# Optimization experiments

Measured on AMD Instinct MI355X. Metric: run time of the kernel, lower is better.

## Reference

```python
import jax, jax.numpy as jnp
import numpy as np


def setup_inputs() -> dict:
    key = jax.random.key(0)
    k1, k2, k3 = jax.random.split(key, 3)
    Lq, Lkv, H, D = 2048, 2048, 16, 128
    return {
        "query": jax.random.normal(k1, (Lq, H, D), dtype=jnp.float32),
        "key": jax.random.normal(k2, (Lkv, H, D), dtype=jnp.float32),
        "value": jax.random.normal(k3, (Lkv, H, D), dtype=jnp.float32),
    }


def reference(query, key, value):
    # query: [Lq, H, D], key: [Lkv, H, D], value: [Lkv, H, Dv]
    # Original module performs chunked online-softmax attention; the math is
    # exactly scaled-dot-product softmax attention with scale 1/sqrt(k_features).
    d = query.shape[-1]
    q = query * (1.0 / jnp.sqrt(jnp.asarray(d, dtype=query.dtype)))
    scores = jnp.einsum('qhd,khd->qhk', q, key)          # [Lq, H, Lkv]
    weights = jax.nn.softmax(scores, axis=-1)            # numerically stable online softmax equivalent
    out = jnp.einsum('qhk,khf->qhf', weights, value)     # [Lq, H, Dv]
    return out
```

## Files before the change

kernel.cpp:

```cpp
#include <hip/hip_runtime.h>
#include <hip/hip_bf16.h>

typedef __bf16 bf16x8 __attribute__((ext_vector_type(8)));
typedef __bf16 bf16x4 __attribute__((ext_vector_type(4)));
typedef float  f32x16 __attribute__((ext_vector_type(16)));
typedef float  f32x4  __attribute__((ext_vector_type(4)));

#define HD     2048
#define DH     128
#define KVB    32
#define NSPLIT 2
#define NROWS  32768
#define VSTR   36

template<bool SPLIT>
__global__ __launch_bounds__(256, 2)
void fmha_kern(const float* __restrict__ Qg, const float* __restrict__ Kg,
               const float* __restrict__ Vg, float* __restrict__ outp,
               float* __restrict__ wsML)
{
    __shared__ __align__(16) __bf16 klds[2][32 * 128];
    __shared__ __align__(16) __bf16 vtlds[2][DH * VSTR];

    const int tid  = threadIdx.x;
    const int lane = tid & 63;
    const int wrp  = tid >> 6;
    const int g    = lane >> 5;
    const int l31  = lane & 31;

    const int b = blockIdx.x;
    int h, qblk, sp, t0, nch;
    if constexpr (SPLIT) {
        const int grp = b & 31;
        qblk = b >> 5;
        h    = grp >> 1;
        sp   = grp & 1;
        t0   = sp * 32;
        nch  = 32;
    } else {
        h    = 2 * (b & 7) + ((b >> 3) >> 4);
        qblk = (b >> 3) & 15;
        sp   = 0;
        t0   = 0;
        nch  = 64;
    }

    const float qscale = 1.4426950408889634f * 0.08838834764831845f;
    const int q = qblk * 128 + wrp * 32 + l31;

    bf16x8 qf[8];
    {
        const float* qrow = Qg + (size_t)q * HD + h * DH;
        #pragma unroll
        for (int db = 0; db < 8; ++db) {
            f32x4 a = *(const f32x4*)(qrow + db * 16 + 8 * g);
            f32x4 c = *(const f32x4*)(qrow + db * 16 + 8 * g + 4);
            bf16x8 f;
            f[0] = (__bf16)(a[0] * qscale); f[1] = (__bf16)(a[1] * qscale);
            f[2] = (__bf16)(a[2] * qscale); f[3] = (__bf16)(a[3] * qscale);
            f[4] = (__bf16)(c[0] * qscale); f[5] = (__bf16)(c[1] * qscale);
            f[6] = (__bf16)(c[2] * qscale); f[7] = (__bf16)(c[3] * qscale);
            qf[db] = f;
        }
    }

    const int krow = tid >> 3, kc = tid & 7;
    const int vkv  = tid & 31, vdv0 = (tid >> 5) * 16;
    const float* kbase = Kg + (size_t)h * DH;
    const float* vbase = Vg + (size_t)h * DH;

    f32x4 kreg0, kreg1, kreg2, kreg3, vreg0, vreg1, vreg2, vreg3;

    auto stage_load = [&](int t) {
        const float* kp = kbase + (size_t)(t * KVB + krow) * HD + kc * 8;
        kreg0 = *(const f32x4*)(kp);
        kreg1 = *(const f32x4*)(kp + 4);
        kreg2 = *(const f32x4*)(kp + 64);
        kreg3 = *(const f32x4*)(kp + 68);
        const float* vp = vbase + (size_t)(t * KVB + vkv) * HD + vdv0;
        vreg0 = *(const f32x4*)(vp);
        vreg1 = *(const f32x4*)(vp + 4);
        vreg2 = *(const f32x4*)(vp + 8);
        vreg3 = *(const f32x4*)(vp + 12);
    };

    auto stage_write = [&](int buf) {
        bf16x8 k0, k1;
        k0[0]=(__bf16)kreg0[0]; k0[1]=(__bf16)kreg0[1]; k0[2]=(__bf16)kreg0[2]; k0[3]=(__bf16)kreg0[3];
        k0[4]=(__bf16)kreg1[0]; k0[5]=(__bf16)kreg1[1]; k0[6]=(__bf16)kreg1[2]; k0[7]=(__bf16)kreg1[3];
        k1[0]=(__bf16)kreg2[0]; k1[1]=(__bf16)kreg2[1]; k1[2]=(__bf16)kreg2[2]; k1[3]=(__bf16)kreg2[3];
        k1[4]=(__bf16)kreg3[0]; k1[5]=(__bf16)kreg3[1]; k1[6]=(__bf16)kreg3[2]; k1[7]=(__bf16)kreg3[3];
        const int swz = (krow & 7) << 3;
        *(bf16x8*)&klds[buf][krow * 128 + ((kc * 8) ^ swz)]      = k0;
        *(bf16x8*)&klds[buf][krow * 128 + ((kc * 8 + 64) ^ swz)] = k1;
        #pragma unroll
        for (int jj = 0; jj < 4; ++jj) {
            f32x4 vv = (jj == 0) ? vreg0 : (jj == 1) ? vreg1 : (jj == 2) ? vreg2 : vreg3;
            #pragma unroll
            for (int e = 0; e < 4; ++e)
                vtlds[buf][(vdv0 + jj * 4 + e) * VSTR + vkv] = (__bf16)vv[e];
        }
    };

    auto block_sync = []() {
        asm volatile("s_waitcnt lgkmcnt(0)" ::: "memory");
        __builtin_amdgcn_s_barrier();
    };

    float mrun = -1e30f, lrun = 0.0f;
    f32x16 o0, o1, o2, o3;
    #pragma unroll
    for (int r = 0; r < 16; ++r) { o0[r] = 0.f; o1[r] = 0.f; o2[r] = 0.f; o3[r] = 0.f; }

    stage_load(t0);
    stage_write(0);
    stage_load(t0 + 1);
    block_sync();

    #pragma unroll 2
    for (int tt = 0; tt < nch; ++tt) {
        const int cur = tt & 1;

        f32x16 sa, sb;
        #pragma unroll
        for (int r = 0; r < 16; ++r) { sa[r] = 0.f; sb[r] = 0.f; }
        const int kswz = (l31 & 7) << 3;
        #pragma unroll
        for (int db = 0; db < 4; ++db) {
            bf16x8 kfa = *(const bf16x8*)&klds[cur][l31 * 128 + (((2*db)   * 16 + g * 8) ^ kswz)];
            sa = __builtin_amdgcn_mfma_f32_32x32x16_bf16(kfa, qf[2*db],   sa, 0, 0, 0);
            bf16x8 kfb = *(const bf16x8*)&klds[cur][l31 * 128 + (((2*db+1) * 16 + g * 8) ^ kswz)];
            sb = __builtin_amdgcn_mfma_f32_32x32x16_bf16(kfb, qf[2*db+1], sb, 0, 0, 0);
        }
        f32x16 s;
        #pragma unroll
        for (int r = 0; r < 16; ++r) s[r] = sa[r] + sb[r];

        float m8[8];
        #pragma unroll
        for (int r = 0; r < 8; ++r) m8[r] = fmaxf(s[r], s[r + 8]);
        float tmax = fmaxf(fmaxf(fmaxf(m8[0], m8[4]), fmaxf(m8[1], m8[5])),
                           fmaxf(fmaxf(m8[2], m8[6]), fmaxf(m8[3], m8[7])));
        tmax = fmaxf(tmax, __shfl_xor(tmax, 32, 64));

        if (__any(tmax > mrun + 8.0f)) {
            const float mnew  = fmaxf(mrun, tmax);
            const float alpha = __builtin_amdgcn_exp2f(mrun - mnew);
            lrun *= alpha;
            #pragma unroll
            for (int r = 0; r < 16; ++r) { o0[r] *= alpha; o1[r] *= alpha; o2[r] *= alpha; o3[r] *= alpha; }
            mrun = mnew;
        }

        float p[16];
        #pragma unroll
        for (int r = 0; r < 16; ++r) p[r] = __builtin_amdgcn_exp2f(s[r] - mrun);
        float ps0 = 0, ps1 = 0, ps2 = 0, ps3 = 0;
        #pragma unroll
        for (int r = 0; r < 4; ++r) { ps0 += p[r]; ps1 += p[r+4]; ps2 += p[r+8]; ps3 += p[r+12]; }
        lrun += ((ps0 + ps1) + (ps2 + ps3));

        bf16x8 pf0, pf1;
        #pragma unroll
        for (int e = 0; e < 8; ++e) { pf0[e] = (__bf16)p[e]; pf1[e] = (__bf16)p[8 + e]; }

        #pragma unroll
        for (int bb = 0; bb < 4; ++bb) {
            const __bf16* vb = &vtlds[cur][(bb * 32 + l31) * VSTR];
            bf16x4 a0 = *(const bf16x4*)(vb + 4 * g);
            bf16x4 a1 = *(const bf16x4*)(vb + 8 + 4 * g);
            bf16x8 va;
            va[0]=a0[0]; va[1]=a0[1]; va[2]=a0[2]; va[3]=a0[3];
            va[4]=a1[0]; va[5]=a1[1]; va[6]=a1[2]; va[7]=a1[3];
            f32x16& oo = (bb == 0) ? o0 : (bb == 1) ? o1 : (bb == 2) ? o2 : o3;
            oo = __builtin_amdgcn_mfma_f32_32x32x16_bf16(va, pf0, oo, 0, 0, 0);
            bf16x4 b0 = *(const bf16x4*)(vb + 16 + 4 * g);
            bf16x4 b1 = *(const bf16x4*)(vb + 24 + 4 * g);
            va[0]=b0[0]; va[1]=b0[1]; va[2]=b0[2]; va[3]=b0[3];
            va[4]=b1[0]; va[5]=b1[1]; va[6]=b1[2]; va[7]=b1[3];
            oo = __builtin_amdgcn_mfma_f32_32x32x16_bf16(va, pf1, oo, 0, 0, 0);
        }

        if (tt + 1 < nch) {
            stage_write(cur ^ 1);
            if (tt + 2 < nch) stage_load(t0 + tt + 2);
            block_sync();
        }
    }

    const float ltot  = lrun + __shfl_xor(lrun, 32, 64);
    const int   rowid = q * 16 + h;

    if constexpr (SPLIT) {
        float* orow = outp + ((size_t)sp * NROWS + rowid) * 128;
        #pragma unroll
        for (int bb = 0; bb < 4; ++bb) {
            const f32x16& oo = (bb == 0) ? o0 : (bb == 1) ? o1 : (bb == 2) ? o2 : o3;
            #pragma unroll
            for (int jj = 0; jj < 4; ++jj) {
                f32x4 v;
                v[0] = oo[4*jj+0]; v[1] = oo[4*jj+1]; v[2] = oo[4*jj+2]; v[3] = oo[4*jj+3];
                *(f32x4*)(orow + bb * 32 + 8 * jj + 4 * g) = v;
            }
        }
        if (lane < 32) {
            float* ml = wsML + ((size_t)sp * NROWS + rowid) * 2;
            ml[0] = mrun;
            ml[1] = ltot;
        }
    } else {
        const float inv = 1.0f / ltot;
        float* orow = outp + (size_t)rowid * 128;
        #pragma unroll
        for (int bb = 0; bb < 4; ++bb) {
            const f32x16& oo = (bb == 0) ? o0 : (bb == 1) ? o1 : (bb == 2) ? o2 : o3;
            #pragma unroll
            for (int jj = 0; jj < 4; ++jj) {
                f32x4 v;
                v[0] = oo[4*jj+0] * inv; v[1] = oo[4*jj+1] * inv;
                v[2] = oo[4*jj+2] * inv; v[3] = oo[4*jj+3] * inv;
                *(f32x4*)(orow + bb * 32 + 8 * jj + 4 * g) = v;
            }
        }
    }
}

__global__ __launch_bounds__(256, 4)
void fmha_combine(const float* __restrict__ wsO, const float* __restrict__ wsML,
                  float* __restrict__ Og)
{
    const int tid   = threadIdx.x;
    const int rowid = blockIdx.x * 8 + (tid >> 5);
    const int c     = (tid & 31) * 4;

    float m[NSPLIT], l[NSPLIT];
    float M = -1e30f;
    #pragma unroll
    for (int s = 0; s < NSPLIT; ++s) {
        const float* ml = wsML + ((size_t)s * NROWS + rowid) * 2;
        m[s] = ml[0];
        l[s] = ml[1];
        M = fmaxf(M, m[s]);
    }
    float L = 0.f, w[NSPLIT];
    #pragma unroll
    for (int s = 0; s < NSPLIT; ++s) {
        w[s] = __builtin_amdgcn_exp2f(m[s] - M);
        L += l[s] * w[s];
    }
    const float inv = 1.0f / L;

    f32x4 acc; acc[0] = 0.f; acc[1] = 0.f; acc[2] = 0.f; acc[3] = 0.f;
    #pragma unroll
    for (int s = 0; s < NSPLIT; ++s) {
        f32x4 v = *(const f32x4*)(wsO + ((size_t)s * NROWS + rowid) * 128 + c);
        acc[0] += v[0] * w[s]; acc[1] += v[1] * w[s];
        acc[2] += v[2] * w[s]; acc[3] += v[3] * w[s];
    }
    f32x4 r;
    r[0] = acc[0] * inv; r[1] = acc[1] * inv; r[2] = acc[2] * inv; r[3] = acc[3] * inv;
    *(f32x4*)(Og + (size_t)rowid * 128 + c) = r;
}

extern "C" void kernel_launch(void* const* d_in, const int* in_sizes, int n_in,
                              void* d_out, int out_size, void* d_ws, size_t ws_size,
                              hipStream_t stream) {
    const float* Q = (const float*)d_in[0];
    const float* K = (const float*)d_in[1];
    const float* V = (const float*)d_in[2];
    float* O = (float*)d_out;

    const size_t needO  = (size_t)NSPLIT * NROWS * 128;
    const size_t needML = (size_t)NSPLIT * NROWS * 2;
    const size_t need_bytes = (needO + needML) * sizeof(float);

    if (ws_size >= need_bytes) {
        float* wsO  = (float*)d_ws;
        float* wsML = wsO + needO;
        hipLaunchKernelGGL(fmha_kern<true>, dim3(512), dim3(256), 0, stream,
                           Q, K, V, wsO, wsML);
        hipLaunchKernelGGL(fmha_combine, dim3(NROWS / 8), dim3(256), 0, stream,
                           wsO, wsML, O);
    } else {
        hipLaunchKernelGGL(fmha_kern<false>, dim3(256), dim3(256), 0, stream,
                           Q, K, V, O, (float*)nullptr);
    }
}
```

Baseline: 73.60 us.

## Widen attention tiles to 256 queries and 64-key chunks with 8 waves

The split-KV kernel now runs 512-thread blocks covering 256 queries and processes 64 keys per chunk instead of 32. This halves the number of K/V staging rounds and barriers and doubles the reuse of each staged tile. The kernel also adds s_setprio around the MFMA sections, moves the LDS write and next global load of the following chunk to right after QK^T so they overlap softmax and PV, and skips rescaling unless the running max grows by more than 8. In exchange the grid drops to 256 blocks, which lowers CU occupancy and parallelism, and register and LDS pressure per block rises.

```diff
diff --git a/kernel.cpp b/kernel.cpp
--- a/kernel.cpp
+++ b/kernel.cpp
@@ -3,23 +3,24 @@
 
 typedef __bf16 bf16x8 __attribute__((ext_vector_type(8)));
 typedef __bf16 bf16x4 __attribute__((ext_vector_type(4)));
+typedef __bf16 bf16x2 __attribute__((ext_vector_type(2)));
 typedef float  f32x16 __attribute__((ext_vector_type(16)));
 typedef float  f32x4  __attribute__((ext_vector_type(4)));
 
 #define HD     2048
 #define DH     128
-#define KVB    32
+#define KVT    64
+#define NCH    16
 #define NSPLIT 2
 #define NROWS  32768
-#define VSTR   36
-
-template<bool SPLIT>
-__global__ __launch_bounds__(256, 2)
+#define VSTR   68
+
+__global__ __launch_bounds__(512, 2)
 void fmha_kern(const float* __restrict__ Qg, const float* __restrict__ Kg,
-               const float* __restrict__ Vg, float* __restrict__ outp,
+               const float* __restrict__ Vg, float* __restrict__ wsO,
                float* __restrict__ wsML)
 {
-    __shared__ __align__(16) __bf16 klds[2][32 * 128];
+    __shared__ __align__(16) __bf16 klds[2][KVT * 128];
     __shared__ __align__(16) __bf16 vtlds[2][DH * VSTR];
 
     const int tid  = threadIdx.x;
@@ -28,22 +29,249 @@
     const int g    = lane >> 5;
     const int l31  = lane & 31;
 
-    const int b = blockIdx.x;
-    int h, qblk, sp, t0, nch;
-    if constexpr (SPLIT) {
-        const int grp = b & 31;
-        qblk = b >> 5;
-        h    = grp >> 1;
-        sp   = grp & 1;
-        t0   = sp * 32;
-        nch  = 32;
-    } else {
-        h    = 2 * (b & 7) + ((b >> 3) >> 4);
-        qblk = (b >> 3) & 15;
-        sp   = 0;
-        t0   = 0;
-        nch  = 64;
-    }
+    const int b    = blockIdx.x;
+    const int grp  = b & 31;
+    const int qblk = b >> 5;
+    const int h    = grp >> 1;
+    const int sp   = grp & 1;
+    const int t0   = sp * NCH;
+
+    const float qscale = 1.4426950408889634f * 0.08838834764831845f;
+    const int q = qblk * 256 + wrp * 32 + l31;
+
+    bf16x8 qf[8];
+    {
+        const float* qrow = Qg + (size_t)q * HD + h * DH;
+        #pragma unroll
+        for (int j = 0; j < 8; ++j) {
+            f32x4 a = *(const f32x4*)(qrow + j * 16 + 8 * g);
+            f32x4 c = *(const f32x4*)(qrow + j * 16 + 8 * g + 4);
+            bf16x8 f;
+            f[0] = (__bf16)(a[0] * qscale); f[1] = (__bf16)(a[1] * qscale);
+            f[2] = (__bf16)(a[2] * qscale); f[3] = (__bf16)(a[3] * qscale);
+            f[4] = (__bf16)(c[0] * qscale); f[5] = (__bf16)(c[1] * qscale);
+            f[6] = (__bf16)(c[2] * qscale); f[7] = (__bf16)(c[3] * qscale);
+            qf[j] = f;
+        }
+    }
+
+    const int krow = tid >> 3, kc = tid & 7;
+    const int kvp  = tid & 31, vdv0 = (tid >> 5) * 8;
+    const float* kbase = Kg + (size_t)h * DH;
+    const float* vbase = Vg + (size_t)h * DH;
+
+    f32x4 kreg0, kreg1, kreg2, kreg3, vreg0, vreg1, vreg2, vreg3;
+
+    auto stage_load = [&](int t) {
+        const float* kp = kbase + (size_t)(t * KVT + krow) * HD + kc * 8;
+        kreg0 = *(const f32x4*)(kp);
+        kreg1 = *(const f32x4*)(kp + 4);
+        kreg2 = *(const f32x4*)(kp + 64);
+        kreg3 = *(const f32x4*)(kp + 68);
+        const float* vp = vbase + (size_t)(t * KVT + 2 * kvp) * HD + vdv0;
+        vreg0 = *(const f32x4*)(vp);
+        vreg1 = *(const f32x4*)(vp + 4);
+        vreg2 = *(const f32x4*)(vp + HD);
+        vreg3 = *(const f32x4*)(vp + HD + 4);
+    };
+
+    auto stage_write = [&](int buf) {
+        bf16x8 k0, k1;
+        k0[0]=(__bf16)kreg0[0]; k0[1]=(__bf16)kreg0[1]; k0[2]=(__bf16)kreg0[2]; k0[3]=(__bf16)kreg0[3];
+        k0[4]=(__bf16)kreg1[0]; k0[5]=(__bf16)kreg1[1]; k0[6]=(__bf16)kreg1[2]; k0[7]=(__bf16)kreg1[3];
+        k1[0]=(__bf16)kreg2[0]; k1[1]=(__bf16)kreg2[1]; k1[2]=(__bf16)kreg2[2]; k1[3]=(__bf16)kreg2[3];
+        k1[4]=(__bf16)kreg3[0]; k1[5]=(__bf16)kreg3[1]; k1[6]=(__bf16)kreg3[2]; k1[7]=(__bf16)kreg3[3];
+        const int swz = (krow & 7) << 3;
+        *(bf16x8*)&klds[buf][krow * 128 + ((kc * 8) ^ swz)]      = k0;
+        *(bf16x8*)&klds[buf][krow * 128 + ((kc * 8 + 64) ^ swz)] = k1;
+        #pragma unroll
+        for (int e = 0; e < 8; ++e) {
+            bf16x2 w;
+            w[0] = (__bf16)((e < 4) ? vreg0[e & 3] : vreg1[e & 3]);
+            w[1] = (__bf16)((e < 4) ? vreg2[e & 3] : vreg3[e & 3]);
+            *(bf16x2*)&vtlds[buf][(vdv0 + e) * VSTR + 2 * kvp] = w;
+        }
+    };
+
+    auto block_sync = []() {
+        asm volatile("s_waitcnt lgkmcnt(0)" ::: "memory");
+        __builtin_amdgcn_s_barrier();
+    };
+
+    float mrun = -1e30f, lrun = 0.0f;
+    f32x16 o0, o1, o2, o3;
+    #pragma unroll
+    for (int r = 0; r < 16; ++r) { o0[r] = 0.f; o1[r] = 0.f; o2[r] = 0.f; o3[r] = 0.f; }
+
+    stage_load(t0);
+    stage_write(0);
+    stage_load(t0 + 1);
+    block_sync();
+
+    const int kswz = (l31 & 7) << 3;
+
+    #pragma unroll 2
+    for (int tt = 0; tt < NCH; ++tt) {
+        const int cur = tt & 1;
+
+        f32x16 s0, s1;
+        #pragma unroll
+        for (int r = 0; r < 16; ++r) { s0[r] = 0.f; s1[r] = 0.f; }
+        __builtin_amdgcn_s_setprio(1);
+        #pragma unroll
+        for (int j = 0; j < 8; ++j) {
+            bf16x8 kf0 = *(const bf16x8*)&klds[cur][l31 * 128 + ((j * 16 + 8 * g) ^ kswz)];
+            s0 = __builtin_amdgcn_mfma_f32_32x32x16_bf16(kf0, qf[j], s0, 0, 0, 0);
+            bf16x8 kf1 = *(const bf16x8*)&klds[cur][(32 + l31) * 128 + ((j * 16 + 8 * g) ^ kswz)];
+            s1 = __builtin_amdgcn_mfma_f32_32x32x16_bf16(kf1, qf[j], s1, 0, 0, 0);
+        }
+        __builtin_amdgcn_s_setprio(0);
+
+        if (tt + 1 < NCH) stage_write(cur ^ 1);
+        if (tt + 2 < NCH) stage_load(t0 + tt + 2);
+
+        float m16[8];
+        #pragma unroll
+        for (int r = 0; r < 8; ++r)
+            m16[r] = fmaxf(fmaxf(s0[r], s0[r + 8]), fmaxf(s1[r], s1[r + 8]));
+        float tmax = fmaxf(fmaxf(fmaxf(m16[0], m16[4]), fmaxf(m16[1], m16[5])),
+                           fmaxf(fmaxf(m16[2], m16[6]), fmaxf(m16[3], m16[7])));
+        tmax = fmaxf(tmax, __shfl_xor(tmax, 32, 64));
+
+        if (__any(tmax > mrun + 8.0f)) {
+            const float mnew  = fmaxf(mrun, tmax);
+            const float alpha = __builtin_amdgcn_exp2f(mrun - mnew);
+            lrun *= alpha;
+            #pragma unroll
+            for (int r = 0; r < 16; ++r) { o0[r] *= alpha; o1[r] *= alpha; o2[r] *= alpha; o3[r] *= alpha; }
+            mrun = mnew;
+        }
+
+        float p0[16], p1[16];
+        #pragma unroll
+        for (int r = 0; r < 16; ++r) {
+            p0[r] = __builtin_amdgcn_exp2f(s0[r] - mrun);
+            p1[r] = __builtin_amdgcn_exp2f(s1[r] - mrun);
+        }
+        float ps = 0.f;
+        #pragma unroll
+        for (int r = 0; r < 16; ++r) ps += p0[r] + p1[r];
+        lrun += ps;
+
+        bf16x8 pfa0, pfa1, pfb0, pfb1;
+        #pragma unroll
+        for (int e = 0; e < 8; ++e) {
+            pfa0[e] = (__bf16)p0[e]; pfa1[e] = (__bf16)p0[8 + e];
+            pfb0[e] = (__bf16)p1[e]; pfb1[e] = (__bf16)p1[8 + e];
+        }
+
+        __builtin_amdgcn_s_setprio(1);
+        #pragma unroll
+        for (int bb = 0; bb < 4; ++bb) {
+            const __bf16* vb = &vtlds[cur][(bb * 32 + l31) * VSTR];
+            f32x16& oo = (bb == 0) ? o0 : (bb == 1) ? o1 : (bb == 2) ? o2 : o3;
+            bf16x8 va;
+            bf16x4 a0, a1;
+            a0 = *(const bf16x4*)(vb + 4 * g);
+            a1 = *(const bf16x4*)(vb + 8 + 4 * g);
+            va[0]=a0[0]; va[1]=a0[1]; va[2]=a0[2]; va[3]=a0[3];
+            va[4]=a1[0]; va[5]=a1[1]; va[6]=a1[2]; va[7]=a1[3];
+            oo = __builtin_amdgcn_mfma_f32_32x32x16_bf16(va, pfa0, oo, 0, 0, 0);
+            a0 = *(const bf16x4*)(vb + 16 + 4 * g);
+            a1 = *(const bf16x4*)(vb + 24 + 4 * g);
+            va[0]=a0[0]; va[1]=a0[1]; va[2]=a0[2]; va[3]=a0[3];
+            va[4]=a1[0]; va[5]=a1[1]; va[6]=a1[2]; va[7]=a1[3];
+            oo = __builtin_amdgcn_mfma_f32_32x32x16_bf16(va, pfa1, oo, 0, 0, 0);
+            a0 = *(const bf16x4*)(vb + 32 + 4 * g);
+            a1 = *(const bf16x4*)(vb + 40 + 4 * g);
+            va[0]=a0[0]; va[1]=a0[1]; va[2]=a0[2]; va[3]=a0[3];
+            va[4]=a1[0]; va[5]=a1[1]; va[6]=a1[2]; va[7]=a1[3];
+            oo = __builtin_amdgcn_mfma_f32_32x32x16_bf16(va, pfb0, oo, 0, 0, 0);
+            a0 = *(const bf16x4*)(vb + 48 + 4 * g);
+            a1 = *(const bf16x4*)(vb + 56 + 4 * g);
+            va[0]=a0[0]; va[1]=a0[1]; va[2]=a0[2]; va[3]=a0[3];
+            va[4]=a1[0]; va[5]=a1[1]; va[6]=a1[2]; va[7]=a1[3];
+            oo = __builtin_amdgcn_mfma_f32_32x32x16_bf16(va, pfb1, oo, 0, 0, 0);
+        }
+        __builtin_amdgcn_s_setprio(0);
+
+        if (tt + 1 < NCH) block_sync();
+    }
+
+    const float ltot  = lrun + __shfl_xor(lrun, 32, 64);
+    const int   rowid = q * 16 + h;
+
+    float* orow = wsO + ((size_t)sp * NROWS + rowid) * 128;
+    #pragma unroll
+    for (int bb = 0; bb < 4; ++bb) {
+        const f32x16& oo = (bb == 0) ? o0 : (bb == 1) ? o1 : (bb == 2) ? o2 : o3;
+        #pragma unroll
+        for (int jj = 0; jj < 4; ++jj) {
+            f32x4 v;
+            v[0] = oo[4*jj+0]; v[1] = oo[4*jj+1]; v[2] = oo[4*jj+2]; v[3] = oo[4*jj+3];
+            *(f32x4*)(orow + bb * 32 + 8 * jj + 4 * g) = v;
+        }
+    }
+    if (lane < 32) {
+        float* ml = wsML + ((size_t)sp * NROWS + rowid) * 2;
+        ml[0] = mrun;
+        ml[1] = ltot;
+    }
+}
+
+__global__ __launch_bounds__(256, 4)
+void fmha_combine(const float* __restrict__ wsO, const float* __restrict__ wsML,
+                  float* __restrict__ Og)
+{
+    const int tid   = threadIdx.x;
+    const int rowid = blockIdx.x * 8 + (tid >> 5);
+    const int c     = (tid & 31) * 4;
+
+    float m[NSPLIT], l[NSPLIT];
+    float M = -1e30f;
+    #pragma unroll
+    for (int s = 0; s < NSPLIT; ++s) {
+        const float* ml = wsML + ((size_t)s * NROWS + rowid) * 2;
+        m[s] = ml[0];
+        l[s] = ml[1];
+        M = fmaxf(M, m[s]);
+    }
+    float L = 0.f, w[NSPLIT];
+    #pragma unroll
+    for (int s = 0; s < NSPLIT; ++s) {
+        w[s] = __builtin_amdgcn_exp2f(m[s] - M);
+        L += l[s] * w[s];
+    }
+    const float inv = 1.0f / L;
+
+    f32x4 acc; acc[0] = 0.f; acc[1] = 0.f; acc[2] = 0.f; acc[3] = 0.f;
+    #pragma unroll
+    for (int s = 0; s < NSPLIT; ++s) {
+        f32x4 v = *(const f32x4*)(wsO + ((size_t)s * NROWS + rowid) * 128 + c);
+        acc[0] += v[0] * w[s]; acc[1] += v[1] * w[s];
+        acc[2] += v[2] * w[s]; acc[3] += v[3] * w[s];
+    }
+    f32x4 r;
+    r[0] = acc[0] * inv; r[1] = acc[1] * inv; r[2] = acc[2] * inv; r[3] = acc[3] * inv;
+    *(f32x4*)(Og + (size_t)rowid * 128 + c) = r;
+}
+
+__global__ __launch_bounds__(256, 2)
+void fmha_fb(const float* __restrict__ Qg, const float* __restrict__ Kg,
+             const float* __restrict__ Vg, float* __restrict__ Og)
+{
+    __shared__ __align__(16) __bf16 klds[2][32 * 128];
+    __shared__ __align__(16) __bf16 vtlds[2][DH * 36];
+
+    const int tid  = threadIdx.x;
+    const int lane = tid & 63;
+    const int wrp  = tid >> 6;
+    const int g    = lane >> 5;
+    const int l31  = lane & 31;
+
+    const int b    = blockIdx.x;
+    const int h    = 2 * (b & 7) + ((b >> 3) >> 4);
+    const int qblk = (b >> 3) & 15;
 
     const float qscale = 1.4426950408889634f * 0.08838834764831845f;
     const int q = qblk * 128 + wrp * 32 + l31;
@@ -72,12 +300,12 @@
     f32x4 kreg0, kreg1, kreg2, kreg3, vreg0, vreg1, vreg2, vreg3;
 
     auto stage_load = [&](int t) {
-        const float* kp = kbase + (size_t)(t * KVB + krow) * HD + kc * 8;
+        const float* kp = kbase + (size_t)(t * 32 + krow) * HD + kc * 8;
         kreg0 = *(const f32x4*)(kp);
         kreg1 = *(const f32x4*)(kp + 4);
         kreg2 = *(const f32x4*)(kp + 64);
         kreg3 = *(const f32x4*)(kp + 68);
-        const float* vp = vbase + (size_t)(t * KVB + vkv) * HD + vdv0;
+        const float* vp = vbase + (size_t)(t * 32 + vkv) * HD + vdv0;
         vreg0 = *(const f32x4*)(vp);
         vreg1 = *(const f32x4*)(vp + 4);
         vreg2 = *(const f32x4*)(vp + 8);
@@ -98,13 +326,8 @@
             f32x4 vv = (jj == 0) ? vreg0 : (jj == 1) ? vreg1 : (jj == 2) ? vreg2 : vreg3;
             #pragma unroll
             for (int e = 0; e < 4; ++e)
-                vtlds[buf][(vdv0 + jj * 4 + e) * VSTR + vkv] = (__bf16)vv[e];
-        }
-    };
-
-    auto block_sync = []() {
-        asm volatile("s_waitcnt lgkmcnt(0)" ::: "memory");
-        __builtin_amdgcn_s_barrier();
+                vtlds[buf][(vdv0 + jj * 4 + e) * 36 + vkv] = (__bf16)vv[e];
+        }
     };
 
     float mrun = -1e30f, lrun = 0.0f;
@@ -112,14 +335,13 @@
     #pragma unroll
     for (int r = 0; r < 16; ++r) { o0[r] = 0.f; o1[r] = 0.f; o2[r] = 0.f; o3[r] = 0.f; }
 
-    stage_load(t0);
+    stage_load(0);
     stage_write(0);
-    stage_load(t0 + 1);
-    block_sync();
-
-    #pragma unroll 2
-    for (int tt = 0; tt < nch; ++tt) {
+
+    for (int tt = 0; tt < 64; ++tt) {
         const int cur = tt & 1;
+        if (tt + 1 < 64) stage_load(tt + 1);
+        __syncthreads();
 
         f32x16 sa, sb;
         #pragma unroll
@@ -166,7 +388,7 @@
 
         #pragma unroll
         for (int bb = 0; bb < 4; ++bb) {
-            const __bf16* vb = &vtlds[cur][(bb * 32 + l31) * VSTR];
+            const __bf16* vb = &vtlds[cur][(bb * 32 + l31) * 36];
             bf16x4 a0 = *(const bf16x4*)(vb + 4 * g);
             bf16x4 a1 = *(const bf16x4*)(vb + 8 + 4 * g);
             bf16x8 va;
@@ -181,85 +403,23 @@
             oo = __builtin_amdgcn_mfma_f32_32x32x16_bf16(va, pf1, oo, 0, 0, 0);
         }
 
-        if (tt + 1 < nch) {
-            stage_write(cur ^ 1);
-            if (tt + 2 < nch) stage_load(t0 + tt + 2);
-            block_sync();
-        }
-    }
-
-    const float ltot  = lrun + __shfl_xor(lrun, 32, 64);
-    const int   rowid = q * 16 + h;
-
-    if constexpr (SPLIT) {
-        float* orow = outp + ((size_t)sp * NROWS + rowid) * 128;
-        #pragma unroll
-        for (int bb = 0; bb < 4; ++bb) {
-            const f32x16& oo = (bb == 0) ? o0 : (bb == 1) ? o1 : (bb == 2) ? o2 : o3;
-            #pragma unroll
-            for (int jj = 0; jj < 4; ++jj) {
-                f32x4 v;
-                v[0] = oo[4*jj+0]; v[1] = oo[4*jj+1]; v[2] = oo[4*jj+2]; v[3] = oo[4*jj+3];
-                *(f32x4*)(orow + bb * 32 + 8 * jj + 4 * g) = v;
-            }
-        }
-        if (lane < 32) {
-            float* ml = wsML + ((size_t)sp * NROWS + rowid) * 2;
-            ml[0] = mrun;
-            ml[1] = ltot;
-        }
-    } else {
-        const float inv = 1.0f / ltot;
-        float* orow = outp + (size_t)rowid * 128;
-        #pragma unroll
-        for (int bb = 0; bb < 4; ++bb) {
-            const f32x16& oo = (bb == 0) ? o0 : (bb == 1) ? o1 : (bb == 2) ? o2 : o3;
-            #pragma unroll
-            for (int jj = 0; jj < 4; ++jj) {
-                f32x4 v;
-                v[0] = oo[4*jj+0] * inv; v[1] = oo[4*jj+1] * inv;
-                v[2] = oo[4*jj+2] * inv; v[3] = oo[4*jj+3] * inv;
-                *(f32x4*)(orow + bb * 32 + 8 * jj + 4 * g) = v;
-            }
-        }
-    }
-}
-
-__global__ __launch_bounds__(256, 4)
-void fmha_combine(const float* __restrict__ wsO, const float* __restrict__ wsML,
-                  float* __restrict__ Og)
-{
-    const int tid   = threadIdx.x;
-    const int rowid = blockIdx.x * 8 + (tid >> 5);
-    const int c     = (tid & 31) * 4;
-
-    float m[NSPLIT], l[NSPLIT];
-    float M = -1e30f;
-    #pragma unroll
-    for (int s = 0; s < NSPLIT; ++s) {
-        const float* ml = wsML + ((size_t)s * NROWS + rowid) * 2;
-        m[s] = ml[0];
-        l[s] = ml[1];
-        M = fmaxf(M, m[s]);
-    }
-    float L = 0.f, w[NSPLIT];
-    #pragma unroll
-    for (int s = 0; s < NSPLIT; ++s) {
-        w[s] = __builtin_amdgcn_exp2f(m[s] - M);
-        L += l[s] * w[s];
-    }
-    const float inv = 1.0f / L;
-
-    f32x4 acc; acc[0] = 0.f; acc[1] = 0.f; acc[2] = 0.f; acc[3] = 0.f;
-    #pragma unroll
-    for (int s = 0; s < NSPLIT; ++s) {
-        f32x4 v = *(const f32x4*)(wsO + ((size_t)s * NROWS + rowid) * 128 + c);
-        acc[0] += v[0] * w[s]; acc[1] += v[1] * w[s];
-        acc[2] += v[2] * w[s]; acc[3] += v[3] * w[s];
-    }
-    f32x4 r;
-    r[0] = acc[0] * inv; r[1] = acc[1] * inv; r[2] = acc[2] * inv; r[3] = acc[3] * inv;
-    *(f32x4*)(Og + (size_t)rowid * 128 + c) = r;
+        if (tt + 1 < 64) stage_write(cur ^ 1);
+    }
+
+    const float ltot = lrun + __shfl_xor(lrun, 32, 64);
+    const float inv  = 1.0f / ltot;
+    float* orow = Og + ((size_t)q * 16 + h) * 128;
+    #pragma unroll
+    for (int bb = 0; bb < 4; ++bb) {
+        const f32x16& oo = (bb == 0) ? o0 : (bb == 1) ? o1 : (bb == 2) ? o2 : o3;
+        #pragma unroll
+        for (int jj = 0; jj < 4; ++jj) {
+            f32x4 v;
+            v[0] = oo[4*jj+0] * inv; v[1] = oo[4*jj+1] * inv;
+            v[2] = oo[4*jj+2] * inv; v[3] = oo[4*jj+3] * inv;
+            *(f32x4*)(orow + bb * 32 + 8 * jj + 4 * g) = v;
+        }
+    }
 }
 
 extern "C" void kernel_launch(void* const* d_in, const int* in_sizes, int n_in,
@@ -277,12 +437,11 @@
     if (ws_size >= need_bytes) {
         float* wsO  = (float*)d_ws;
         float* wsML = wsO + needO;
-        hipLaunchKernelGGL(fmha_kern<true>, dim3(512), dim3(256), 0, stream,
+        hipLaunchKernelGGL(fmha_kern, dim3(256), dim3(512), 0, stream,
                            Q, K, V, wsO, wsML);
         hipLaunchKernelGGL(fmha_combine, dim3(NROWS / 8), dim3(256), 0, stream,
                            wsO, wsML, O);
     } else {
-        hipLaunchKernelGGL(fmha_kern<false>, dim3(256), dim3(256), 0, stream,
-                           Q, K, V, O, (float*)nullptr);
+        hipLaunchKernelGGL(fmha_fb, dim3(256), dim3(256), 0, stream, Q, K, V, O);
     }
 }
```

New measurement: 66.65 us. 1.1x faster.
